# Kernel tuning notes

Hardware: AMD Instinct MI355X
Metric: run time of the kernel (lower is better)

The kernel has to match this reference:

```python
import jax, jax.numpy as jnp
import numpy as np

N = 100000      # nodes
E = 1600000     # edges (before self loops)
IN_F = 128
OUT_F = 32
HEADS = 4
NEG_SLOPE = 0.2


def setup_inputs() -> dict:
    key = jax.random.key(0)
    k1, k2, k3, k4, k5, k6 = jax.random.split(key, 6)
    x = jax.random.normal(k1, (N, IN_F), dtype=jnp.float32)
    edge_index = jax.random.randint(k2, (2, E), 0, N, dtype=jnp.int64)
    # PyG GATConv params: shared linear W [in, H*F], attention vectors att_src/att_dst [1,H,F], bias [H*F]
    glorot = (6.0 / (IN_F + HEADS * OUT_F)) ** 0.5
    W = jax.random.uniform(k3, (IN_F, HEADS * OUT_F), dtype=jnp.float32, minval=-glorot, maxval=glorot)
    ga = (6.0 / (1 + OUT_F)) ** 0.5
    att_src = jax.random.uniform(k4, (HEADS, OUT_F), dtype=jnp.float32, minval=-ga, maxval=ga)
    att_dst = jax.random.uniform(k5, (HEADS, OUT_F), dtype=jnp.float32, minval=-ga, maxval=ga)
    bias = jnp.zeros((HEADS * OUT_F,), dtype=jnp.float32)
    return {"x": x, "edge_index": edge_index, "W": W, "att_src": att_src, "att_dst": att_dst, "bias": bias}


def reference(x, edge_index, W, att_src, att_dst, bias):
    n = x.shape[0]
    # add self loops (PyG add_self_loops=True)
    loops = jnp.arange(n, dtype=edge_index.dtype)
    src = jnp.concatenate([edge_index[0], loops])  # [E+N] message source j
    dst = jnp.concatenate([edge_index[1], loops])  # [E+N] message target i

    h = (x @ W).reshape(n, HEADS, OUT_F)                 # [N,H,F]
    a_src = jnp.sum(h * att_src[None], axis=-1)          # [N,H]
    a_dst = jnp.sum(h * att_dst[None], axis=-1)          # [N,H]

    e = a_src[src] + a_dst[dst]                          # [E',H]
    e = jax.nn.leaky_relu(e, NEG_SLOPE)
    # per-destination softmax over incoming edges
    m = jax.ops.segment_max(e, dst, num_segments=n)      # [N,H]
    ex = jnp.exp(e - m[dst])
    s = jax.ops.segment_sum(ex, dst, num_segments=n)     # [N,H]
    alpha = ex / (s[dst] + 1e-16)                        # [E',H]

    msg = h[src] * alpha[:, :, None]                     # [E',H,F]
    out = jax.ops.segment_sum(msg, dst, num_segments=n)  # [N,H,F]
    return out.reshape(n, HEADS * OUT_F) + bias
```

## Files before the change

kernel.cpp:

```cpp
#include <hip/hip_runtime.h>


#define NEG_SLOPE 0.2f
#define NB_MAX 256
#define BSHIFT 9
#define CHUNK 4096
#define BCAP 12288
#define CAP 11264
#define SS_STRIDE 11520
#define LOG2E 1.4426950408889634f

typedef __attribute__((ext_vector_type(8))) short short8;
typedef __attribute__((ext_vector_type(4))) float f32x4;
typedef __attribute__((ext_vector_type(2))) float f32x2;

__device__ __forceinline__ unsigned int rne16(unsigned int u) {
  return (u + 0x7fffu + ((u >> 16) & 1u)) >> 16;
}
__device__ __forceinline__ unsigned int f2bf_pack(float a, float b) {
  return (rne16(__float_as_uint(b)) << 16) | (rne16(__float_as_uint(a)) & 0xffffu);
}

__global__ __launch_bounds__(256) void k_prep(
    const float* __restrict__ W, unsigned short* __restrict__ Wt,
    int* __restrict__ bcnt) {
  int tid = threadIdx.x;
  if (blockIdx.x == 64) { bcnt[tid] = 0; return; }
  int idx = blockIdx.x * 256 + tid;
  int k = idx >> 7, col = idx & 127;
  Wt[col * 128 + k] = (unsigned short)rne16(__float_as_uint(W[idx]));
}

__device__ __forceinline__ void gemm_tile(
    int gbid, int tid, int Nn,
    const float* __restrict__ x, const unsigned short* __restrict__ Wt,
    unsigned int* __restrict__ hb,
    const float* __restrict__ attS, const float* __restrict__ attD,
    float* __restrict__ aS, float* __restrict__ aD) {
  int w = tid >> 6, lane = tid & 63;
  int m = lane & 15, q = lane >> 4;
  int r0 = gbid * 64 + w * 16;
  int rowA = r0 + m; if (rowA >= Nn) rowA = Nn - 1;
  const float* xrow = x + (unsigned)rowA * 128u;

  f32x4 acc[8];
#pragma unroll
  for (int t = 0; t < 8; ++t) acc[t] = (f32x4){0.f, 0.f, 0.f, 0.f};

#pragma unroll
  for (int ks = 0; ks < 4; ++ks) {
    int k0 = ks * 32 + q * 8;
    float4 a0 = *(const float4*)(xrow + k0);
    float4 a1 = *(const float4*)(xrow + k0 + 4);
    unsigned au[4];
    au[0] = f2bf_pack(a0.x, a0.y);
    au[1] = f2bf_pack(a0.z, a0.w);
    au[2] = f2bf_pack(a1.x, a1.y);
    au[3] = f2bf_pack(a1.z, a1.w);
    short8 af = *(short8*)au;
#pragma unroll
    for (int t = 0; t < 8; ++t) {
      short8 bf = *(const short8*)(Wt + (unsigned)(t * 16 + m) * 128u + k0);
      acc[t] = __builtin_amdgcn_mfma_f32_16x16x32_bf16(af, bf, acc[t], 0, 0, 0);
    }
  }

  float sSa[4], sSb[4], sDa[4], sDb[4];
#pragma unroll
  for (int u = 0; u < 4; ++u) {
    sSa[u] = attS[u * 32 + m]; sSb[u] = attS[u * 32 + m + 16];
    sDa[u] = attD[u * 32 + m]; sDb[u] = attD[u * 32 + m + 16];
  }

#pragma unroll
  for (int r = 0; r < 4; ++r) {
    int rowo = r0 + q * 4 + r;
    bool ok = rowo < Nn;
    if (ok) {
#pragma unroll
      for (int u = 0; u < 4; ++u)
        hb[(unsigned)rowo * 64u + u * 16 + m] = f2bf_pack(acc[2 * u][r], acc[2 * u + 1][r]);
    }
#pragma unroll
    for (int u = 0; u < 4; ++u) {
      float pS = acc[2 * u][r] * sSa[u] + acc[2 * u + 1][r] * sSb[u];
      float pD = acc[2 * u][r] * sDa[u] + acc[2 * u + 1][r] * sDb[u];
#pragma unroll
      for (int d = 8; d >= 1; d >>= 1) {
        pS += __shfl_down(pS, d, 16);
        pD += __shfl_down(pD, d, 16);
      }
      if (ok && m == 0) {
        aS[(unsigned)rowo * 4u + u] = pS * LOG2E;
        aD[(unsigned)rowo * 4u + u] = pD * LOG2E;
      }
    }
  }
}

__global__ __launch_bounds__(256) void k_binmm(
    const int* __restrict__ ei, int* __restrict__ bcnt,
    unsigned int* __restrict__ binned, int E, int Nn, int nb, int nbBin,
    const float* __restrict__ x, const unsigned short* __restrict__ Wt,
    unsigned int* __restrict__ hb,
    const float* __restrict__ attS, const float* __restrict__ attD,
    float* __restrict__ aS, float* __restrict__ aD) {
  __shared__ unsigned int buf[CHUNK];
  __shared__ unsigned char bkt[CHUNK];
  __shared__ int hist[NB_MAX];
  __shared__ int loc[NB_MAX];
  __shared__ int gbase[NB_MAX];
  int tid = threadIdx.x;

  if ((int)blockIdx.x >= nbBin) {
    gemm_tile(blockIdx.x - nbBin, tid, Nn, x, Wt, hb, attS, attD, aS, aD);
    return;
  }

  int e0 = blockIdx.x * CHUNK;
  int n = E - e0; if (n > CHUNK) n = CHUNK;

  hist[tid] = 0;
  __syncthreads();

  int dstv[CHUNK / 256];
  int srcv[CHUNK / 256];
  int rankv[CHUNK / 256];
#pragma unroll
  for (int j = 0; j < CHUNK / 256; ++j) {
    int idx = j * 256 + tid;
    dstv[j] = -1;
    if (idx < n) {
      int d = ei[E + e0 + idx];
      srcv[j] = ei[e0 + idx];
      dstv[j] = d;
      rankv[j] = atomicAdd(&hist[d >> BSHIFT], 1);
    }
  }
  __syncthreads();

  if (tid < 64) {
    int base = tid * 4;
    int v0 = hist[base], v1 = hist[base + 1], v2 = hist[base + 2], v3 = hist[base + 3];
    int s = v0 + v1 + v2 + v3;
    int inc = s;
#pragma unroll
    for (int d = 1; d < 64; d <<= 1) {
      int t = __shfl_up(inc, d, 64);
      if (tid >= d) inc += t;
    }
    int ex = inc - s;
    loc[base] = ex; loc[base + 1] = ex + v0;
    loc[base + 2] = ex + v0 + v1; loc[base + 3] = ex + v0 + v1 + v2;
  }
  __syncthreads();

#pragma unroll
  for (int j = 0; j < CHUNK / 256; ++j) {
    if (dstv[j] >= 0) {
      int b = dstv[j] >> BSHIFT;
      int slot = loc[b] + rankv[j];
      buf[slot] = (unsigned)srcv[j] | ((unsigned)(dstv[j] & 511) << 20);
      bkt[slot] = (unsigned char)b;
    }
  }
  for (int b = tid; b < nb; b += 256)
    if (hist[b] > 0) gbase[b] = atomicAdd(&bcnt[b], hist[b]);
  __syncthreads();

  for (int s = tid; s < n; s += 256) {
    int b = bkt[s];
    binned[(unsigned)b * BCAP + gbase[b] + (s - loc[b])] = buf[s];
  }
}

__global__ __launch_bounds__(512) void k_scatgemm(
    const unsigned int* __restrict__ binned, const int* __restrict__ bcnt,
    int2* __restrict__ off2, int* __restrict__ ssrc, int Nn, int nb, int nGemmA,
    const float* __restrict__ x, const unsigned short* __restrict__ Wt,
    unsigned int* __restrict__ hb,
    const float* __restrict__ attS, const float* __restrict__ attD,
    float* __restrict__ aS, float* __restrict__ aD) {
  __shared__ int cnt[512];
  __shared__ int obuf[CAP];
  __shared__ int wsum[8];
  int b = blockIdx.x, tid = threadIdx.x;

  if (b >= nb) {
    gemm_tile(nGemmA + (b - nb) * 2 + (tid >> 8), tid & 255, Nn,
              x, Wt, hb, attS, attD, aS, aD);
    return;
  }

  int node0 = b << BSHIFT;
  int nnodes = Nn - node0; if (nnodes > 512) nnodes = 512;
  int nE = bcnt[b];
  const unsigned* bp = binned + (unsigned)b * BCAP;

  cnt[tid] = 0;
  __syncthreads();
  int nE4 = nE >> 2;
  for (int i = tid; i < nE4; i += 512) {
    uint4 p = *(const uint4*)(bp + 4 * i);
    atomicAdd(&cnt[(p.x >> 20) & 511u], 1);
    atomicAdd(&cnt[(p.y >> 20) & 511u], 1);
    atomicAdd(&cnt[(p.z >> 20) & 511u], 1);
    atomicAdd(&cnt[(p.w >> 20) & 511u], 1);
  }
  for (int i = (nE4 << 2) + tid; i < nE; i += 512)
    atomicAdd(&cnt[(bp[i] >> 20) & 511u], 1);
  __syncthreads();

  int v = cnt[tid] + (tid < nnodes ? 1 : 0);
  int lane = tid & 63, w = tid >> 6;
  int inc = v;
#pragma unroll
  for (int d = 1; d < 64; d <<= 1) {
    int t = __shfl_up(inc, d, 64);
    if (lane >= d) inc += t;
  }
  if (lane == 63) wsum[w] = inc;
  __syncthreads();
  int wbase = 0;
  for (int ww = 0; ww < w; ++ww) wbase += wsum[ww];
  int ex = wbase + inc - v;
  __syncthreads();

  int csrBase = b * SS_STRIDE;
  if (tid < nnodes) {
    off2[node0 + tid] = make_int2(csrBase + ex, v);
    obuf[ex] = node0 + tid;
  }
  cnt[tid] = ex + 1;
  __syncthreads();

  for (int i = tid; i < nE4; i += 512) {
    uint4 p = *(const uint4*)(bp + 4 * i);
    { int d = (p.x >> 20) & 511u; int pos = atomicAdd(&cnt[d], 1); if (pos < CAP) obuf[pos] = (int)(p.x & 0xFFFFFu); }
    { int d = (p.y >> 20) & 511u; int pos = atomicAdd(&cnt[d], 1); if (pos < CAP) obuf[pos] = (int)(p.y & 0xFFFFFu); }
    { int d = (p.z >> 20) & 511u; int pos = atomicAdd(&cnt[d], 1); if (pos < CAP) obuf[pos] = (int)(p.z & 0xFFFFFu); }
    { int d = (p.w >> 20) & 511u; int pos = atomicAdd(&cnt[d], 1); if (pos < CAP) obuf[pos] = (int)(p.w & 0xFFFFFu); }
  }
  for (int i = (nE4 << 2) + tid; i < nE; i += 512) {
    unsigned p = bp[i];
    int d = (p >> 20) & 511u;
    int pos = atomicAdd(&cnt[d], 1);
    if (pos < CAP) obuf[pos] = (int)(p & 0xFFFFFu);
  }
  __syncthreads();

  int tot = nE + nnodes;
  int tot4 = tot >> 2;
  for (int i = tid; i < tot4; i += 512)
    *(int4*)(ssrc + csrBase + 4 * i) = *(const int4*)(obuf + 4 * i);
  for (int i = (tot4 << 2) + tid; i < tot; i += 512)
    ssrc[csrBase + i] = obuf[i];
}

__global__ __launch_bounds__(256) void k_aggregate(
    const unsigned int* __restrict__ hb, const float* __restrict__ aS, const float* __restrict__ aD,
    const int2* __restrict__ off2, const int* __restrict__ ssrc,
    const float* __restrict__ bias, float* __restrict__ out, int Nn) {
  int wave = threadIdx.x >> 6;
  int lane = threadIdx.x & 63;
  int node = blockIdx.x * 4 + wave;
  if (node >= Nn) return;
  int un = __builtin_amdgcn_readfirstlane(node);
  unsigned hd = (unsigned)lane >> 4;
  float ad = aD[(unsigned)un * 4u + hd];
  int2 o = off2[un];
  int p0 = o.x;
  int deg = o.y;
  const int* sp = ssrc + p0;
  int nch = deg >> 2;
  f32x2 acc = {0.f, 0.f};
  float denA = 0.f, denB = 0.f;

  int s0 = 0, s1 = 0, s2 = 0, s3 = 0;
  unsigned v0 = 0, v1 = 0, v2 = 0, v3 = 0;
  float a0 = 0.f, a1 = 0.f, a2 = 0.f, a3 = 0.f;
  if (nch > 0) {
    s0 = sp[0]; s1 = sp[1]; s2 = sp[2]; s3 = sp[3];
    v0 = hb[(unsigned)s0 * 64u + lane]; v1 = hb[(unsigned)s1 * 64u + lane];
    v2 = hb[(unsigned)s2 * 64u + lane]; v3 = hb[(unsigned)s3 * 64u + lane];
    a0 = aS[(unsigned)s0 * 4u + hd]; a1 = aS[(unsigned)s1 * 4u + hd];
    a2 = aS[(unsigned)s2 * 4u + hd]; a3 = aS[(unsigned)s3 * 4u + hd];
    sp += 4;
  }
  for (int c = 0; c < nch; ++c) {
    int t0 = 0, t1 = 0, t2 = 0, t3 = 0;
    unsigned w0 = 0, w1 = 0, w2 = 0, w3 = 0;
    float b0 = 0.f, b1 = 0.f, b2 = 0.f, b3 = 0.f;
    if (c + 1 < nch) {
      t0 = sp[0]; t1 = sp[1]; t2 = sp[2]; t3 = sp[3];
      w0 = hb[(unsigned)t0 * 64u + lane]; w1 = hb[(unsigned)t1 * 64u + lane];
      w2 = hb[(unsigned)t2 * 64u + lane]; w3 = hb[(unsigned)t3 * 64u + lane];
      b0 = aS[(unsigned)t0 * 4u + hd]; b1 = aS[(unsigned)t1 * 4u + hd];
      b2 = aS[(unsigned)t2 * 4u + hd]; b3 = aS[(unsigned)t3 * 4u + hd];
      sp += 4;
    }
    float e0 = a0 + ad, e1 = a1 + ad, e2 = a2 + ad, e3 = a3 + ad;
    e0 = fmaxf(e0, NEG_SLOPE * e0); e1 = fmaxf(e1, NEG_SLOPE * e1);
    e2 = fmaxf(e2, NEG_SLOPE * e2); e3 = fmaxf(e3, NEG_SLOPE * e3);
    float x0 = exp2f(e0), x1 = exp2f(e1), x2 = exp2f(e2), x3 = exp2f(e3);
    denA += x0 + x1; denB += x2 + x3;
    f32x2 h0 = { __uint_as_float(v0 << 16), __uint_as_float(v0 & 0xffff0000u) };
    f32x2 h1 = { __uint_as_float(v1 << 16), __uint_as_float(v1 & 0xffff0000u) };
    f32x2 h2 = { __uint_as_float(v2 << 16), __uint_as_float(v2 & 0xffff0000u) };
    f32x2 h3 = { __uint_as_float(v3 << 16), __uint_as_float(v3 & 0xffff0000u) };
    acc = h0 * x0 + acc;
    acc = h1 * x1 + acc;
    acc = h2 * x2 + acc;
    acc = h3 * x3 + acc;
    s0 = t0; s1 = t1; s2 = t2; s3 = t3;
    v0 = w0; v1 = w1; v2 = w2; v3 = w3;
    a0 = b0; a1 = b1; a2 = b2; a3 = b3;
  }
  for (int p = nch << 2; p < deg; ++p) {
    int src = (ssrc + p0)[p];
    float e = aS[(unsigned)src * 4u + hd] + ad;
    e = fmaxf(e, NEG_SLOPE * e);
    float ex = exp2f(e);
    unsigned v = hb[(unsigned)src * 64u + lane];
    f32x2 hh = { __uint_as_float(v << 16), __uint_as_float(v & 0xffff0000u) };
    acc = hh * ex + acc;
    denA += ex;
  }
  float inv = 1.0f / (denA + denB + 1e-16f);
  unsigned col = hd * 32u + ((unsigned)lane & 15u);
  out[(unsigned)un * 128u + col] = acc.x * inv + bias[col];
  out[(unsigned)un * 128u + col + 16u] = acc.y * inv + bias[col + 16];
}

extern "C" void kernel_launch(void* const* d_in, const int* in_sizes, int n_in,
                              void* d_out, int out_size, void* d_ws, size_t ws_size,
                              hipStream_t stream) {
  const float* x    = (const float*)d_in[0];
  const int*   ei   = (const int*)d_in[1];
  const float* W    = (const float*)d_in[2];
  const float* attS = (const float*)d_in[3];
  const float* attD = (const float*)d_in[4];
  const float* bias = (const float*)d_in[5];
  float* out = (float*)d_out;

  const int Nn = in_sizes[0] / 128;
  const int E  = in_sizes[1] / 2;
  const int nb = (Nn + (1 << BSHIFT) - 1) >> BSHIFT;
  const int nbBin = (E + CHUNK - 1) / CHUNK;
  const int nGemm = (Nn + 63) / 64;
  const int nGemmA = (nGemm * 2) / 3;
  const int nGemmB = nGemm - nGemmA;
  const int nFill = (nGemmB + 1) / 2;

  char* ws = (char*)d_ws;
  size_t o = 0;
  auto take = [&](size_t bytes) { void* p = ws + o; o += (bytes + 255) & ~(size_t)255; return p; };
  int2* off2     = (int2*)take((size_t)(Nn + 1) * 8);
  int* ssrc      = (int*)take((size_t)NB_MAX * SS_STRIDE * 4);
  int* bcnt      = (int*)take((size_t)NB_MAX * 4);
  float* aS      = (float*)take((size_t)Nn * 4 * 4);
  float* aD      = (float*)take((size_t)Nn * 4 * 4);
  unsigned short* Wt = (unsigned short*)take((size_t)128 * 128 * 2);
  unsigned int* hb = (unsigned int*)take((size_t)Nn * 64 * 4);
  unsigned int* binned = (unsigned int*)take((size_t)NB_MAX * BCAP * 4);
  (void)ws_size; (void)o;

  k_prep<<<65, 256, 0, stream>>>(W, Wt, bcnt);
  k_binmm<<<nbBin + nGemmA, 256, 0, stream>>>(ei, bcnt, binned, E, Nn, nb, nbBin,
                                              x, Wt, hb, attS, attD, aS, aD);
  k_scatgemm<<<nb + nFill, 512, 0, stream>>>(binned, bcnt, off2, ssrc, Nn, nb,
                                             nGemmA, x, Wt, hb, attS, attD, aS, aD);
  k_aggregate<<<(Nn + 3) / 4, 256, 0, stream>>>(hb, aS, aD, off2, ssrc, bias, out, Nn);
}
```

Baseline: 240.7 us.

## Scatter binned edges and CSR directly to global memory, drop LDS staging

The binning kernel no longer builds a locally sorted chunk in shared memory. Each edge now goes straight to its global bin slot, computed as the global base plus its local rank. The CSR scatter kernel also writes source ids directly into the global ssrc array instead of staging them in a large LDS buffer and copying them out. That kernel moves to 1024-thread blocks with four GEMM tiles per fill block, and the GEMM split between the two kernels is rebalanced. The aim is to cut LDS use and extra passes so occupancy can rise, at the cost of uncoalesced scattered global writes and dropping the CAP overflow guard.

```diff
diff --git a/kernel.cpp b/kernel.cpp
--- a/kernel.cpp
+++ b/kernel.cpp
@@ -6,7 +6,6 @@
 #define BSHIFT 9
 #define CHUNK 4096
 #define BCAP 12288
-#define CAP 11264
 #define SS_STRIDE 11520
 #define LOG2E 1.4426950408889634f
 
@@ -105,10 +104,7 @@
     unsigned int* __restrict__ hb,
     const float* __restrict__ attS, const float* __restrict__ attD,
     float* __restrict__ aS, float* __restrict__ aD) {
-  __shared__ unsigned int buf[CHUNK];
-  __shared__ unsigned char bkt[CHUNK];
   __shared__ int hist[NB_MAX];
-  __shared__ int loc[NB_MAX];
   __shared__ int gbase[NB_MAX];
   int tid = threadIdx.x;
 
@@ -139,42 +135,20 @@
   }
   __syncthreads();
 
-  if (tid < 64) {
-    int base = tid * 4;
-    int v0 = hist[base], v1 = hist[base + 1], v2 = hist[base + 2], v3 = hist[base + 3];
-    int s = v0 + v1 + v2 + v3;
-    int inc = s;
-#pragma unroll
-    for (int d = 1; d < 64; d <<= 1) {
-      int t = __shfl_up(inc, d, 64);
-      if (tid >= d) inc += t;
-    }
-    int ex = inc - s;
-    loc[base] = ex; loc[base + 1] = ex + v0;
-    loc[base + 2] = ex + v0 + v1; loc[base + 3] = ex + v0 + v1 + v2;
-  }
+  if (hist[tid] > 0) gbase[tid] = atomicAdd(&bcnt[tid], hist[tid]);
   __syncthreads();
 
 #pragma unroll
   for (int j = 0; j < CHUNK / 256; ++j) {
     if (dstv[j] >= 0) {
       int b = dstv[j] >> BSHIFT;
-      int slot = loc[b] + rankv[j];
-      buf[slot] = (unsigned)srcv[j] | ((unsigned)(dstv[j] & 511) << 20);
-      bkt[slot] = (unsigned char)b;
-    }
-  }
-  for (int b = tid; b < nb; b += 256)
-    if (hist[b] > 0) gbase[b] = atomicAdd(&bcnt[b], hist[b]);
-  __syncthreads();
-
-  for (int s = tid; s < n; s += 256) {
-    int b = bkt[s];
-    binned[(unsigned)b * BCAP + gbase[b] + (s - loc[b])] = buf[s];
-  }
-}
-
-__global__ __launch_bounds__(512) void k_scatgemm(
+      binned[(unsigned)b * BCAP + gbase[b] + rankv[j]] =
+          (unsigned)srcv[j] | ((unsigned)(dstv[j] & 511) << 20);
+    }
+  }
+}
+
+__global__ __launch_bounds__(1024) void k_scatgemm(
     const unsigned int* __restrict__ binned, const int* __restrict__ bcnt,
     int2* __restrict__ off2, int* __restrict__ ssrc, int Nn, int nb, int nGemmA,
     const float* __restrict__ x, const unsigned short* __restrict__ Wt,
@@ -182,12 +156,11 @@
     const float* __restrict__ attS, const float* __restrict__ attD,
     float* __restrict__ aS, float* __restrict__ aD) {
   __shared__ int cnt[512];
-  __shared__ int obuf[CAP];
   __shared__ int wsum[8];
   int b = blockIdx.x, tid = threadIdx.x;
 
   if (b >= nb) {
-    gemm_tile(nGemmA + (b - nb) * 2 + (tid >> 8), tid & 255, Nn,
+    gemm_tile(nGemmA + (b - nb) * 4 + (tid >> 8), tid & 255, Nn,
               x, Wt, hb, attS, attD, aS, aD);
     return;
   }
@@ -196,65 +169,64 @@
   int nnodes = Nn - node0; if (nnodes > 512) nnodes = 512;
   int nE = bcnt[b];
   const unsigned* bp = binned + (unsigned)b * BCAP;
-
-  cnt[tid] = 0;
+  int csrBase = b * SS_STRIDE;
+
+  if (tid < 512) cnt[tid] = 0;
   __syncthreads();
   int nE4 = nE >> 2;
-  for (int i = tid; i < nE4; i += 512) {
+  for (int i = tid; i < nE4; i += 1024) {
     uint4 p = *(const uint4*)(bp + 4 * i);
     atomicAdd(&cnt[(p.x >> 20) & 511u], 1);
     atomicAdd(&cnt[(p.y >> 20) & 511u], 1);
     atomicAdd(&cnt[(p.z >> 20) & 511u], 1);
     atomicAdd(&cnt[(p.w >> 20) & 511u], 1);
   }
-  for (int i = (nE4 << 2) + tid; i < nE; i += 512)
+  for (int i = (nE4 << 2) + tid; i < nE; i += 1024)
     atomicAdd(&cnt[(bp[i] >> 20) & 511u], 1);
   __syncthreads();
 
-  int v = cnt[tid] + (tid < nnodes ? 1 : 0);
-  int lane = tid & 63, w = tid >> 6;
-  int inc = v;
-#pragma unroll
-  for (int d = 1; d < 64; d <<= 1) {
-    int t = __shfl_up(inc, d, 64);
-    if (lane >= d) inc += t;
-  }
-  if (lane == 63) wsum[w] = inc;
-  __syncthreads();
-  int wbase = 0;
-  for (int ww = 0; ww < w; ++ww) wbase += wsum[ww];
-  int ex = wbase + inc - v;
-  __syncthreads();
-
-  int csrBase = b * SS_STRIDE;
-  if (tid < nnodes) {
+  int ex = 0, v = 0;
+  if (tid < 512) {
+    v = cnt[tid] + (tid < nnodes ? 1 : 0);
+    int lane = tid & 63, w = tid >> 6;
+    int inc = v;
+#pragma unroll
+    for (int d = 1; d < 64; d <<= 1) {
+      int t = __shfl_up(inc, d, 64);
+      if (lane >= d) inc += t;
+    }
+    if (lane == 63) wsum[w] = inc;
+    ex = inc - v;
+  }
+  __syncthreads();
+  if (tid < 512) {
+    int w = tid >> 6;
+    int wbase = 0;
+    for (int ww = 0; ww < w; ++ww) wbase += wsum[ww];
+    ex += wbase;
+  }
+  __syncthreads();
+
+  if (tid < 512 && tid < nnodes) {
     off2[node0 + tid] = make_int2(csrBase + ex, v);
-    obuf[ex] = node0 + tid;
-  }
-  cnt[tid] = ex + 1;
-  __syncthreads();
-
-  for (int i = tid; i < nE4; i += 512) {
+    ssrc[csrBase + ex] = node0 + tid;
+  }
+  if (tid < 512) cnt[tid] = ex + 1;
+  __syncthreads();
+
+  for (int i = tid; i < nE4; i += 1024) {
     uint4 p = *(const uint4*)(bp + 4 * i);
-    { int d = (p.x >> 20) & 511u; int pos = atomicAdd(&cnt[d], 1); if (pos < CAP) obuf[pos] = (int)(p.x & 0xFFFFFu); }
-    { int d = (p.y >> 20) & 511u; int pos = atomicAdd(&cnt[d], 1); if (pos < CAP) obuf[pos] = (int)(p.y & 0xFFFFFu); }
-    { int d = (p.z >> 20) & 511u; int pos = atomicAdd(&cnt[d], 1); if (pos < CAP) obuf[pos] = (int)(p.z & 0xFFFFFu); }
-    { int d = (p.w >> 20) & 511u; int pos = atomicAdd(&cnt[d], 1); if (pos < CAP) obuf[pos] = (int)(p.w & 0xFFFFFu); }
-  }
-  for (int i = (nE4 << 2) + tid; i < nE; i += 512) {
+    { int d = (p.x >> 20) & 511u; int pos = atomicAdd(&cnt[d], 1); ssrc[csrBase + pos] = (int)(p.x & 0xFFFFFu); }
+    { int d = (p.y >> 20) & 511u; int pos = atomicAdd(&cnt[d], 1); ssrc[csrBase + pos] = (int)(p.y & 0xFFFFFu); }
+    { int d = (p.z >> 20) & 511u; int pos = atomicAdd(&cnt[d], 1); ssrc[csrBase + pos] = (int)(p.z & 0xFFFFFu); }
+    { int d = (p.w >> 20) & 511u; int pos = atomicAdd(&cnt[d], 1); ssrc[csrBase + pos] = (int)(p.w & 0xFFFFFu); }
+  }
+  for (int i = (nE4 << 2) + tid; i < nE; i += 1024) {
     unsigned p = bp[i];
     int d = (p >> 20) & 511u;
     int pos = atomicAdd(&cnt[d], 1);
-    if (pos < CAP) obuf[pos] = (int)(p & 0xFFFFFu);
-  }
-  __syncthreads();
-
-  int tot = nE + nnodes;
-  int tot4 = tot >> 2;
-  for (int i = tid; i < tot4; i += 512)
-    *(int4*)(ssrc + csrBase + 4 * i) = *(const int4*)(obuf + 4 * i);
-  for (int i = (tot4 << 2) + tid; i < tot; i += 512)
-    ssrc[csrBase + i] = obuf[i];
+    ssrc[csrBase + pos] = (int)(p & 0xFFFFFu);
+  }
 }
 
 __global__ __launch_bounds__(256) void k_aggregate(
@@ -348,9 +320,9 @@
   const int nb = (Nn + (1 << BSHIFT) - 1) >> BSHIFT;
   const int nbBin = (E + CHUNK - 1) / CHUNK;
   const int nGemm = (Nn + 63) / 64;
-  const int nGemmA = (nGemm * 2) / 3;
+  const int nGemmA = nGemm / 2;
   const int nGemmB = nGemm - nGemmA;
-  const int nFill = (nGemmB + 1) / 2;
+  const int nFill = (nGemmB + 3) / 4;
 
   char* ws = (char*)d_ws;
   size_t o = 0;
@@ -368,7 +340,7 @@
   k_prep<<<65, 256, 0, stream>>>(W, Wt, bcnt);
   k_binmm<<<nbBin + nGemmA, 256, 0, stream>>>(ei, bcnt, binned, E, Nn, nb, nbBin,
                                               x, Wt, hb, attS, attD, aS, aD);
-  k_scatgemm<<<nb + nFill, 512, 0, stream>>>(binned, bcnt, off2, ssrc, Nn, nb,
-                                             nGemmA, x, Wt, hb, attS, attD, aS, aD);
+  k_scatgemm<<<nb + nFill, 1024, 0, stream>>>(binned, bcnt, off2, ssrc, Nn, nb,
+                                              nGemmA, x, Wt, hb, attS, attD, aS, aD);
   k_aggregate<<<(Nn + 3) / 4, 256, 0, stream>>>(hb, aS, aD, off2, ssrc, bias, out, Nn);
 }
```

New measurement: 252.0 us. +4.7%, slower.
